# Optimization experiments

Hardware: AMD Instinct MI355X
Metric: run time of the kernel (lower is better)

The kernel has to match this reference:

```python
import jax, jax.numpy as jnp
from jax import lax
import numpy as np

B, N_VARS, M_CLAUSES, K_DIM = 1024, 64, 256, 12
MAX_ITER = 12


def setup_inputs() -> dict:
    key = jax.random.key(0)
    k1, k2, k3, k4 = jax.random.split(key, 4)
    z = jax.random.uniform(k1, (B, N_VARS), dtype=jnp.float32)          # input probabilities
    S = jax.random.normal(k2, (M_CLAUSES, N_VARS + 1), dtype=jnp.float32) * 0.2  # learnable clause matrix (col 0 = truth var)
    w = jax.random.uniform(k3, (M_CLAUSES,), dtype=jnp.float32)          # learnable clause weights
    r = jax.random.normal(k4, (B, N_VARS, K_DIM), dtype=jnp.float32)     # random init directions
    return {"z": z, "S": S, "w": w, "r": r, "max_iter": MAX_ITER}


def _mixing(z, S, w, r, max_iter):
    Bsz, n = z.shape
    m, N = S.shape  # N = n + 1 (truth variable is column 0)
    k = r.shape[-1]
    eps = jnp.float32(1e-8)

    # truth direction v_T = e_0
    vT = jnp.zeros((k,), dtype=z.dtype).at[0].set(1.0)

    # random unit directions orthogonal to v_T (zero out component along e_0)
    r_perp = r.at[..., 0].set(0.0)
    r_perp = r_perp / jnp.maximum(jnp.linalg.norm(r_perp, axis=-1, keepdims=True), eps)

    # SATNet init: v_i = -cos(pi z_i) v_T + sin(pi z_i) r_perp_i
    ang = jnp.pi * z
    Vvars = -jnp.cos(ang)[..., None] * vT + jnp.sin(ang)[..., None] * r_perp  # [B,n,k]
    V = jnp.concatenate([jnp.broadcast_to(vT, (Bsz, 1, k)), Vvars], axis=1)   # [B,N,k]

    Sw = S * w[:, None]                       # weighted clause matrix [m,N]
    W = jnp.einsum('mn,bnk->bmk', Sw, V)      # running product Sw @ V, [B,m,k]
    snrm = jnp.sum(Sw * Sw, axis=0)           # ||s_i||^2 per variable, [N]

    def coord_step(carry, i):
        V, W = carry
        s_i = Sw[:, i]                         # [m]
        v_old = V[:, i, :]                     # [B,k]
        g = jnp.einsum('bmk,m->bk', W, s_i) - snrm[i] * v_old
        v_new = -g / jnp.maximum(jnp.linalg.norm(g, axis=-1, keepdims=True), eps)
        W = W + (v_new - v_old)[:, None, :] * s_i[None, :, None]  # rank-1 update
        V = V.at[:, i, :].set(v_new)
        return (V, W), None

    def sweep(carry, _):
        carry, _ = lax.scan(coord_step, carry, jnp.arange(1, N))  # coordinate descent over variables
        return carry, None

    (V, _), _ = lax.scan(sweep, (V, W), None, length=max_iter)

    # output probabilities: z_i = arccos(-v_i . v_T) / pi
    cos = jnp.clip(-V[:, 1:, 0], -1.0 + 1e-6, 1.0 - 1e-6)
    return jnp.arccos(cos) / jnp.pi


def reference(z, S, w, r, max_iter):
    return _mixing(z, S, w, r, max_iter)
```

## Files before the change

kernel.cpp:

```cpp
#include <hip/hip_runtime.h>
#include <math.h>

#define BATCH 1024
#define NV    64
#define MC    256
#define KD    12
#define PI_F  3.14159265358979323846f

#define C0OFF  4096
#define DGAOFF 4160
#define DGBOFF 4224
#define CBUF   4288

typedef float f2  __attribute__((ext_vector_type(2)));
typedef float v4f __attribute__((ext_vector_type(4)));
typedef __attribute__((address_space(3))) float lds_f;

template <int CTRL>
__device__ __forceinline__ float dpp_addf(float x) {
  int y = __builtin_amdgcn_update_dpp(0, __float_as_int(x), CTRL, 0xF, 0xF, true);
  return x + __int_as_float(y);
}
__device__ __forceinline__ float readlane63(float x) {
  return __int_as_float(__builtin_amdgcn_readlane(__float_as_int(x), 63));
}
__device__ __forceinline__ float rlane(float x, int i) {
  return __int_as_float(__builtin_amdgcn_readlane(__float_as_int(x), i));
}

template <int IMM>
__device__ __forceinline__ void dsr(v4f& d, unsigned base) {
  asm volatile("ds_read_b128 %0, %1 offset:%2" : "=v"(d) : "v"(base), "i"(IMM));
}

__global__ void compute_C_kernel(const float* __restrict__ S,
                                 const float* __restrict__ w,
                                 float* __restrict__ Cg, int nsplit) {
  const int q = blockIdx.x;
  const int mc = blockIdx.y;
  const int j = threadIdx.x;
  if (j > NV) return;
  const int v = (q + 1) % 64 + 1;
  const int mlen = MC / nsplit;
  const int m0 = mc * mlen;
  float a0 = 0.f, a1 = 0.f, a2 = 0.f, a3 = 0.f;
  for (int m = m0; m < m0 + mlen; m += 4) {
    const float w0 = w[m], w1 = w[m + 1], w2 = w[m + 2], w3 = w[m + 3];
    a0 = fmaf(S[(m + 0) * (NV + 1) + v] * w0 * w0, S[(m + 0) * (NV + 1) + j], a0);
    a1 = fmaf(S[(m + 1) * (NV + 1) + v] * w1 * w1, S[(m + 1) * (NV + 1) + j], a1);
    a2 = fmaf(S[(m + 2) * (NV + 1) + v] * w2 * w2, S[(m + 2) * (NV + 1) + j], a2);
    a3 = fmaf(S[(m + 3) * (NV + 1) + v] * w3 * w3, S[(m + 3) * (NV + 1) + j], a3);
  }
  const float acc = (a0 + a1) + (a2 + a3);
  float* buf = Cg + mc * CBUF;
  const int p1 = (v == 1) ? 64 : (v - 1);
  const int p2 = (v == 1) ? 63 : (v == 2) ? 64 : (v - 2);
  if (j == 0) buf[C0OFF + q] = acc;
  if (j == p1) buf[DGAOFF + (v - 1)] = acc;
  if (j == p2) buf[DGBOFF + (v - 1)] = acc;
  if (j > 0) {
    const int j0 = j - 1;
    const float st = (j == v || j == p1 || j == p2) ? 0.f : acc;
    buf[q * 64 + (j0 & 7) * 8 + (j0 >> 3)] = st;
  }
}

__global__ __launch_bounds__(256, 1) void mixing_kernel(
    const float* __restrict__ z, const float* __restrict__ r,
    const float* __restrict__ Cg, const int* __restrict__ max_iter_p,
    float* __restrict__ out, int nsplit) {
  __shared__ __align__(16) float Ls[CBUF];

  const int t = threadIdx.x;
  const int l = t & 63;
  const int jgx = (l & 3) | ((l >> 1) & 4);
  const int kl = ((l >> 2) & 1) | ((l >> 3) & 6);
  const int b = blockIdx.x * 4 + (t >> 6);
  const int max_iter = max_iter_p[0];

  {
    const float4* src = (const float4*)Cg;
    float4* dst = (float4*)Ls;
    for (int idx = t; idx < CBUF / 4; idx += 256) {
      float4 a = src[idx];
      for (int u = 1; u < nsplit; ++u) {
        const float4 p = src[u * (CBUF / 4) + idx];
        a.x += p.x; a.y += p.y; a.z += p.z; a.w += p.w;
      }
      dst[idx] = a;
    }
  }

  const float my_e0 = (kl == 0) ? 1.f : 0.f;

  f2 Vv[8];
  #pragma unroll
  for (int m = 0; m < 8; ++m) {
    const int j0 = jgx + 8 * m;
    const float zv = z[b * NV + j0];
    f2 rp = {0.f, 0.f};
    if (kl < 6) rp = *(const f2*)&r[(b * NV + j0) * KD + 2 * kl];
    if (kl == 0) rp.x = 0.f;
    float ssp = fmaf(rp.x, rp.x, rp.y * rp.y);
    ssp += __shfl_xor(ssp, 4, 64);
    ssp += __shfl_xor(ssp, 16, 64);
    ssp += __shfl_xor(ssp, 32, 64);
    const float inv = 1.f / fmaxf(sqrtf(ssp), 1e-8f);
    const float sn = __builtin_amdgcn_sinf(0.5f * zv);
    const float cs = __builtin_amdgcn_cosf(0.5f * zv);
    const float si = sn * inv;
    Vv[m].x = (kl == 0) ? -cs : si * rp.x;
    Vv[m].y = si * rp.y;
  }

  __syncthreads();

  const float t0v = Ls[C0OFF + l];
  const float t1v = Ls[DGAOFF + l];
  const float t2v = Ls[DGBOFF + l];

  f2 P, vp1, vp2;

  {
    const v4f cA = *(const v4f*)&Ls[63 * 64 + jgx * 8];
    const v4f cB = *(const v4f*)&Ls[63 * 64 + jgx * 8 + 4];
    f2 q = (f2){cA.x, cA.x} * Vv[0];
    q = __builtin_elementwise_fma((f2){cA.y, cA.y}, Vv[1], q);
    q = __builtin_elementwise_fma((f2){cA.z, cA.z}, Vv[2], q);
    q = __builtin_elementwise_fma((f2){cA.w, cA.w}, Vv[3], q);
    q = __builtin_elementwise_fma((f2){cB.x, cB.x}, Vv[4], q);
    q = __builtin_elementwise_fma((f2){cB.y, cB.y}, Vv[5], q);
    q = __builtin_elementwise_fma((f2){cB.z, cB.z}, Vv[6], q);
    q = __builtin_elementwise_fma((f2){cB.w, cB.w}, Vv[7], q);
    q.x = dpp_addf<0xB1>(q.x);  q.y = dpp_addf<0xB1>(q.y);
    q.x = dpp_addf<0x4E>(q.x);  q.y = dpp_addf<0x4E>(q.y);
    q.x = dpp_addf<0x128>(q.x); q.y = dpp_addf<0x128>(q.y);
    q.x = fmaf(my_e0, Ls[C0OFF + 63], q.x);
    P = q;
    vp1.x = __shfl(Vv[7].x, (l & 0x34) | 0x0B, 64);
    vp1.y = __shfl(Vv[7].y, (l & 0x34) | 0x0B, 64);
    vp2.x = __shfl(Vv[7].x, (l & 0x34) | 0x0A, 64);
    vp2.y = __shfl(Vv[7].y, (l & 0x34) | 0x0A, 64);
  }

  const unsigned lbase = (unsigned)(unsigned long long)(lds_f*)&Ls[jgx * 8];

  v4f Rb[4][2];

#define PFROW(R) \
  dsr<((((R) & 63) * 256) + 0)>(Rb[(R) & 3][0], lbase); \
  dsr<((((R) & 63) * 256) + 16)>(Rb[(R) & 3][1], lbase);

#define WAITR(SL) \
  asm volatile("s_waitcnt lgkmcnt(4)" : "+v"(Rb[SL][0]), "+v"(Rb[SL][1]));

#define STEPF(I) { \
  constexpr int i_ = (I); \
  constexpr int s_ = i_ & 3; \
  constexpr int j0w_ = (i_ + 63) & 63; \
  constexpr int m_ = j0w_ >> 3; \
  constexpr int jgo_ = j0w_ & 7; \
  WAITR(s_) \
  PFROW(i_ + 3) \
  const float da_ = rlane(t1v, i_); \
  const float db_ = rlane(t2v, i_); \
  const float c0_ = rlane(t0v, i_); \
   \
  f2 g_; \
  g_.x = fmaf(da_, vp1.x, fmaf(db_, vp2.x, P.x)); \
  g_.y = fmaf(da_, vp1.y, fmaf(db_, vp2.y, P.y)); \
  float t_ = fmaf(g_.x, g_.x, g_.y * g_.y); \
  const v4f ceA = Rb[s_][0], ceB = Rb[s_][1]; \
  f2 q_ = (f2){ceA.x, ceA.x} * Vv[0]; \
  q_ = __builtin_elementwise_fma((f2){ceA.y, ceA.y}, Vv[1], q_); \
  t_ = dpp_addf<0x124>(t_);             \
  q_ = __builtin_elementwise_fma((f2){ceA.z, ceA.z}, Vv[2], q_); \
  q_ = __builtin_elementwise_fma((f2){ceA.w, ceA.w}, Vv[3], q_); \
  t_ = dpp_addf<0x142>(t_);             \
  q_ = __builtin_elementwise_fma((f2){ceB.x, ceB.x}, Vv[4], q_); \
  q_ = __builtin_elementwise_fma((f2){ceB.y, ceB.y}, Vv[5], q_); \
  t_ = dpp_addf<0x143>(t_);             \
  q_ = __builtin_elementwise_fma((f2){ceB.z, ceB.z}, Vv[6], q_); \
  q_ = __builtin_elementwise_fma((f2){ceB.w, ceB.w}, Vv[7], q_); \
  const float n2_ = readlane63(t_); \
  const float inv_ = __builtin_amdgcn_rsqf(fmaxf(n2_, 1e-16f)); \
  q_.x = dpp_addf<0xB1>(q_.x);  q_.y = dpp_addf<0xB1>(q_.y); \
  f2 vn_; vn_.x = -g_.x * inv_; vn_.y = -g_.y * inv_; \
  q_.x = dpp_addf<0x4E>(q_.x);  q_.y = dpp_addf<0x4E>(q_.y); \
  q_.x = dpp_addf<0x128>(q_.x); q_.y = dpp_addf<0x128>(q_.y); \
  q_.x = fmaf(my_e0, c0_, q_.x); \
   \
  Vv[m_].x = (jgx == jgo_) ? vp1.x : Vv[m_].x; \
  Vv[m_].y = (jgx == jgo_) ? vp1.y : Vv[m_].y; \
   \
  vp2 = vp1; vp1 = vn_; P = q_; \
}

#define S4(N) STEPF((N) + 0) STEPF((N) + 1) STEPF((N) + 2) STEPF((N) + 3)
#define S16(N) S4((N) + 0) S4((N) + 4) S4((N) + 8) S4((N) + 12)

  asm volatile("s_waitcnt lgkmcnt(0)" ::: "memory");
  PFROW(0) PFROW(1) PFROW(2)

  #pragma unroll 1
  for (int it = 0; it < max_iter; ++it) {
    S16(0) S16(16) S16(32) S16(48)
  }

  Vv[7].x = (jgx == 7) ? vp1.x : Vv[7].x;
  Vv[7].y = (jgx == 7) ? vp1.y : Vv[7].y;

  asm volatile("s_waitcnt lgkmcnt(0)" ::: "memory");
  __syncthreads();
  {
    float* Lw = Ls + (t >> 6) * 64;
    if (kl == 0) {
      #pragma unroll
      for (int m = 0; m < 8; ++m) Lw[jgx + 8 * m] = Vv[m].x;
    }
    __builtin_amdgcn_s_waitcnt(0);
    float cv = -Lw[l];
    cv = fminf(fmaxf(cv, -1.f + 1e-6f), 1.f - 1e-6f);
    out[b * NV + l] = acosf(cv) * (1.f / PI_F);
  }
}

extern "C" void kernel_launch(void* const* d_in, const int* in_sizes, int n_in,
                              void* d_out, int out_size, void* d_ws, size_t ws_size,
                              hipStream_t stream) {
  const float* z = (const float*)d_in[0];
  const float* S = (const float*)d_in[1];
  const float* w = (const float*)d_in[2];
  const float* r = (const float*)d_in[3];
  const int* max_iter = (const int*)d_in[4];
  float* Cg = (float*)d_ws;

  const int nsplit = (ws_size >= (size_t)8 * CBUF * 4) ? 8
                   : (ws_size >= (size_t)4 * CBUF * 4) ? 4 : 1;
  compute_C_kernel<<<dim3(NV, nsplit), 128, 0, stream>>>(S, w, Cg, nsplit);
  mixing_kernel<<<BATCH / 4, 256, 0, stream>>>(z, r, Cg, max_iter,
                                               (float*)d_out, nsplit);
}
```

Measured before the change: 141.7 us.

## Process two batch elements per wavefront to interleave independent dependency chains

Each wavefront now carries two independent batch problems (A and B) through the coordinate-descent sweep, with their steps interleaved. Blocks shrink from 4 to 2 wavefronts while the grid stays the same. The aim is to hide latency in the serial chain (readlane, rsq, DPP reductions) by giving the scheduler independent work, and to reuse each LDS row read for both problems. The cost is roughly double the VGPR use per wave and half as many waves in flight.

Result: slower. 192.4 us (+35.8%).

```diff
diff --git a/kernel.cpp b/kernel.cpp
--- a/kernel.cpp
+++ b/kernel.cpp
@@ -15,6 +15,11 @@
 typedef float f2  __attribute__((ext_vector_type(2)));
 typedef float v4f __attribute__((ext_vector_type(4)));
 typedef __attribute__((address_space(3))) float lds_f;
+
+__device__ __forceinline__ f2 bc2(float x) { f2 y; y.x = x; y.y = x; return y; }
+__device__ __forceinline__ f2 fma2(f2 a, f2 b, f2 c) {
+  return __builtin_elementwise_fma(a, b, c);
+}
 
 template <int CTRL>
 __device__ __forceinline__ float dpp_addf(float x) {
@@ -65,7 +70,7 @@
   }
 }
 
-__global__ __launch_bounds__(256, 1) void mixing_kernel(
+__global__ __launch_bounds__(128, 1) void mixing_kernel(
     const float* __restrict__ z, const float* __restrict__ r,
     const float* __restrict__ Cg, const int* __restrict__ max_iter_p,
     float* __restrict__ out, int nsplit) {
@@ -75,13 +80,14 @@
   const int l = t & 63;
   const int jgx = (l & 3) | ((l >> 1) & 4);
   const int kl = ((l >> 2) & 1) | ((l >> 3) & 6);
-  const int b = blockIdx.x * 4 + (t >> 6);
+  const int bA = blockIdx.x * 4 + (t >> 6) * 2;
+  const int bB = bA + 1;
   const int max_iter = max_iter_p[0];
 
   {
     const float4* src = (const float4*)Cg;
     float4* dst = (float4*)Ls;
-    for (int idx = t; idx < CBUF / 4; idx += 256) {
+    for (int idx = t; idx < CBUF / 4; idx += 128) {
       float4 a = src[idx];
       for (int u = 1; u < nsplit; ++u) {
         const float4 p = src[u * (CBUF / 4) + idx];
@@ -93,24 +99,30 @@
 
   const float my_e0 = (kl == 0) ? 1.f : 0.f;
 
-  f2 Vv[8];
+  f2 VvA[8], VvB[8];
   #pragma unroll
   for (int m = 0; m < 8; ++m) {
     const int j0 = jgx + 8 * m;
-    const float zv = z[b * NV + j0];
-    f2 rp = {0.f, 0.f};
-    if (kl < 6) rp = *(const f2*)&r[(b * NV + j0) * KD + 2 * kl];
-    if (kl == 0) rp.x = 0.f;
-    float ssp = fmaf(rp.x, rp.x, rp.y * rp.y);
-    ssp += __shfl_xor(ssp, 4, 64);
-    ssp += __shfl_xor(ssp, 16, 64);
-    ssp += __shfl_xor(ssp, 32, 64);
-    const float inv = 1.f / fmaxf(sqrtf(ssp), 1e-8f);
-    const float sn = __builtin_amdgcn_sinf(0.5f * zv);
-    const float cs = __builtin_amdgcn_cosf(0.5f * zv);
-    const float si = sn * inv;
-    Vv[m].x = (kl == 0) ? -cs : si * rp.x;
-    Vv[m].y = si * rp.y;
+    #pragma unroll
+    for (int ab = 0; ab < 2; ++ab) {
+      const int b = ab ? bB : bA;
+      const float zv = z[b * NV + j0];
+      f2 rp = bc2(0.f);
+      if (kl < 6) rp = *(const f2*)&r[(b * NV + j0) * KD + 2 * kl];
+      if (kl == 0) rp.x = 0.f;
+      float ssp = fmaf(rp.x, rp.x, rp.y * rp.y);
+      ssp += __shfl_xor(ssp, 4, 64);
+      ssp += __shfl_xor(ssp, 16, 64);
+      ssp += __shfl_xor(ssp, 32, 64);
+      const float inv = 1.f / fmaxf(sqrtf(ssp), 1e-8f);
+      const float sn = __builtin_amdgcn_sinf(0.5f * zv);
+      const float cs = __builtin_amdgcn_cosf(0.5f * zv);
+      const float si = sn * inv;
+      f2 vv;
+      vv.x = (kl == 0) ? -cs : si * rp.x;
+      vv.y = si * rp.y;
+      if (ab) VvB[m] = vv; else VvA[m] = vv;
+    }
   }
 
   __syncthreads();
@@ -119,28 +131,35 @@
   const float t1v = Ls[DGAOFF + l];
   const float t2v = Ls[DGBOFF + l];
 
-  f2 P, vp1, vp2;
+  f2 PA, PB, vp1A, vp1B, vp2A, vp2B;
 
   {
     const v4f cA = *(const v4f*)&Ls[63 * 64 + jgx * 8];
     const v4f cB = *(const v4f*)&Ls[63 * 64 + jgx * 8 + 4];
-    f2 q = (f2){cA.x, cA.x} * Vv[0];
-    q = __builtin_elementwise_fma((f2){cA.y, cA.y}, Vv[1], q);
-    q = __builtin_elementwise_fma((f2){cA.z, cA.z}, Vv[2], q);
-    q = __builtin_elementwise_fma((f2){cA.w, cA.w}, Vv[3], q);
-    q = __builtin_elementwise_fma((f2){cB.x, cB.x}, Vv[4], q);
-    q = __builtin_elementwise_fma((f2){cB.y, cB.y}, Vv[5], q);
-    q = __builtin_elementwise_fma((f2){cB.z, cB.z}, Vv[6], q);
-    q = __builtin_elementwise_fma((f2){cB.w, cB.w}, Vv[7], q);
-    q.x = dpp_addf<0xB1>(q.x);  q.y = dpp_addf<0xB1>(q.y);
-    q.x = dpp_addf<0x4E>(q.x);  q.y = dpp_addf<0x4E>(q.y);
-    q.x = dpp_addf<0x128>(q.x); q.y = dpp_addf<0x128>(q.y);
-    q.x = fmaf(my_e0, Ls[C0OFF + 63], q.x);
-    P = q;
-    vp1.x = __shfl(Vv[7].x, (l & 0x34) | 0x0B, 64);
-    vp1.y = __shfl(Vv[7].y, (l & 0x34) | 0x0B, 64);
-    vp2.x = __shfl(Vv[7].x, (l & 0x34) | 0x0A, 64);
-    vp2.y = __shfl(Vv[7].y, (l & 0x34) | 0x0A, 64);
+    const float c063 = Ls[C0OFF + 63];
+    #pragma unroll
+    for (int ab = 0; ab < 2; ++ab) {
+      f2* Vv = ab ? VvB : VvA;
+      f2 q = bc2(cA.x) * Vv[0];
+      q = fma2(bc2(cA.y), Vv[1], q);
+      q = fma2(bc2(cA.z), Vv[2], q);
+      q = fma2(bc2(cA.w), Vv[3], q);
+      q = fma2(bc2(cB.x), Vv[4], q);
+      q = fma2(bc2(cB.y), Vv[5], q);
+      q = fma2(bc2(cB.z), Vv[6], q);
+      q = fma2(bc2(cB.w), Vv[7], q);
+      q.x = dpp_addf<0xB1>(q.x);  q.y = dpp_addf<0xB1>(q.y);
+      q.x = dpp_addf<0x4E>(q.x);  q.y = dpp_addf<0x4E>(q.y);
+      q.x = dpp_addf<0x128>(q.x); q.y = dpp_addf<0x128>(q.y);
+      q.x = fmaf(my_e0, c063, q.x);
+      f2 v1, v2;
+      v1.x = __shfl(Vv[7].x, (l & 0x34) | 0x0B, 64);
+      v1.y = __shfl(Vv[7].y, (l & 0x34) | 0x0B, 64);
+      v2.x = __shfl(Vv[7].x, (l & 0x34) | 0x0A, 64);
+      v2.y = __shfl(Vv[7].y, (l & 0x34) | 0x0A, 64);
+      if (ab) { PB = q; vp1B = v1; vp2B = v2; }
+      else    { PA = q; vp1A = v1; vp2A = v2; }
+    }
   }
 
   const unsigned lbase = (unsigned)(unsigned long long)(lds_f*)&Ls[jgx * 8];
@@ -166,34 +185,59 @@
   const float db_ = rlane(t2v, i_); \
   const float c0_ = rlane(t0v, i_); \
    \
-  f2 g_; \
-  g_.x = fmaf(da_, vp1.x, fmaf(db_, vp2.x, P.x)); \
-  g_.y = fmaf(da_, vp1.y, fmaf(db_, vp2.y, P.y)); \
-  float t_ = fmaf(g_.x, g_.x, g_.y * g_.y); \
+  f2 gA_, gB_; \
+  gA_.x = fmaf(da_, vp1A.x, fmaf(db_, vp2A.x, PA.x)); \
+  gB_.x = fmaf(da_, vp1B.x, fmaf(db_, vp2B.x, PB.x)); \
+  gA_.y = fmaf(da_, vp1A.y, fmaf(db_, vp2A.y, PA.y)); \
+  gB_.y = fmaf(da_, vp1B.y, fmaf(db_, vp2B.y, PB.y)); \
+  float tA_ = fmaf(gA_.x, gA_.x, gA_.y * gA_.y); \
+  float tB_ = fmaf(gB_.x, gB_.x, gB_.y * gB_.y); \
   const v4f ceA = Rb[s_][0], ceB = Rb[s_][1]; \
-  f2 q_ = (f2){ceA.x, ceA.x} * Vv[0]; \
-  q_ = __builtin_elementwise_fma((f2){ceA.y, ceA.y}, Vv[1], q_); \
-  t_ = dpp_addf<0x124>(t_);             \
-  q_ = __builtin_elementwise_fma((f2){ceA.z, ceA.z}, Vv[2], q_); \
-  q_ = __builtin_elementwise_fma((f2){ceA.w, ceA.w}, Vv[3], q_); \
-  t_ = dpp_addf<0x142>(t_);             \
-  q_ = __builtin_elementwise_fma((f2){ceB.x, ceB.x}, Vv[4], q_); \
-  q_ = __builtin_elementwise_fma((f2){ceB.y, ceB.y}, Vv[5], q_); \
-  t_ = dpp_addf<0x143>(t_);             \
-  q_ = __builtin_elementwise_fma((f2){ceB.z, ceB.z}, Vv[6], q_); \
-  q_ = __builtin_elementwise_fma((f2){ceB.w, ceB.w}, Vv[7], q_); \
-  const float n2_ = readlane63(t_); \
-  const float inv_ = __builtin_amdgcn_rsqf(fmaxf(n2_, 1e-16f)); \
-  q_.x = dpp_addf<0xB1>(q_.x);  q_.y = dpp_addf<0xB1>(q_.y); \
-  f2 vn_; vn_.x = -g_.x * inv_; vn_.y = -g_.y * inv_; \
-  q_.x = dpp_addf<0x4E>(q_.x);  q_.y = dpp_addf<0x4E>(q_.y); \
-  q_.x = dpp_addf<0x128>(q_.x); q_.y = dpp_addf<0x128>(q_.y); \
-  q_.x = fmaf(my_e0, c0_, q_.x); \
+  f2 qA_ = bc2(ceA.x) * VvA[0]; \
+  f2 qB_ = bc2(ceA.x) * VvB[0]; \
+  qA_ = fma2(bc2(ceA.y), VvA[1], qA_); \
+  qB_ = fma2(bc2(ceA.y), VvB[1], qB_); \
+  tA_ = dpp_addf<0x124>(tA_); \
+  tB_ = dpp_addf<0x124>(tB_); \
+  qA_ = fma2(bc2(ceA.z), VvA[2], qA_); \
+  qB_ = fma2(bc2(ceA.z), VvB[2], qB_); \
+  qA_ = fma2(bc2(ceA.w), VvA[3], qA_); \
+  qB_ = fma2(bc2(ceA.w), VvB[3], qB_); \
+  tA_ = dpp_addf<0x142>(tA_); \
+  tB_ = dpp_addf<0x142>(tB_); \
+  qA_ = fma2(bc2(ceB.x), VvA[4], qA_); \
+  qB_ = fma2(bc2(ceB.x), VvB[4], qB_); \
+  qA_ = fma2(bc2(ceB.y), VvA[5], qA_); \
+  qB_ = fma2(bc2(ceB.y), VvB[5], qB_); \
+  tA_ = dpp_addf<0x143>(tA_); \
+  tB_ = dpp_addf<0x143>(tB_); \
+  qA_ = fma2(bc2(ceB.z), VvA[6], qA_); \
+  qB_ = fma2(bc2(ceB.z), VvB[6], qB_); \
+  qA_ = fma2(bc2(ceB.w), VvA[7], qA_); \
+  qB_ = fma2(bc2(ceB.w), VvB[7], qB_); \
+  const float n2A_ = readlane63(tA_); \
+  const float n2B_ = readlane63(tB_); \
+  const float invA_ = __builtin_amdgcn_rsqf(fmaxf(n2A_, 1e-16f)); \
+  const float invB_ = __builtin_amdgcn_rsqf(fmaxf(n2B_, 1e-16f)); \
+  qA_.x = dpp_addf<0xB1>(qA_.x);  qA_.y = dpp_addf<0xB1>(qA_.y); \
+  qB_.x = dpp_addf<0xB1>(qB_.x);  qB_.y = dpp_addf<0xB1>(qB_.y); \
+  f2 vnA_, vnB_; \
+  vnA_.x = -gA_.x * invA_; vnA_.y = -gA_.y * invA_; \
+  vnB_.x = -gB_.x * invB_; vnB_.y = -gB_.y * invB_; \
+  qA_.x = dpp_addf<0x4E>(qA_.x);  qA_.y = dpp_addf<0x4E>(qA_.y); \
+  qB_.x = dpp_addf<0x4E>(qB_.x);  qB_.y = dpp_addf<0x4E>(qB_.y); \
+  qA_.x = dpp_addf<0x128>(qA_.x); qA_.y = dpp_addf<0x128>(qA_.y); \
+  qB_.x = dpp_addf<0x128>(qB_.x); qB_.y = dpp_addf<0x128>(qB_.y); \
+  qA_.x = fmaf(my_e0, c0_, qA_.x); \
+  qB_.x = fmaf(my_e0, c0_, qB_.x); \
    \
-  Vv[m_].x = (jgx == jgo_) ? vp1.x : Vv[m_].x; \
-  Vv[m_].y = (jgx == jgo_) ? vp1.y : Vv[m_].y; \
+  VvA[m_].x = (jgx == jgo_) ? vp1A.x : VvA[m_].x; \
+  VvA[m_].y = (jgx == jgo_) ? vp1A.y : VvA[m_].y; \
+  VvB[m_].x = (jgx == jgo_) ? vp1B.x : VvB[m_].x; \
+  VvB[m_].y = (jgx == jgo_) ? vp1B.y : VvB[m_].y; \
    \
-  vp2 = vp1; vp1 = vn_; P = q_; \
+  vp2A = vp1A; vp1A = vnA_; PA = qA_; \
+  vp2B = vp1B; vp1B = vnB_; PB = qB_; \
 }
 
 #define S4(N) STEPF((N) + 0) STEPF((N) + 1) STEPF((N) + 2) STEPF((N) + 3)
@@ -207,21 +251,29 @@
     S16(0) S16(16) S16(32) S16(48)
   }
 
-  Vv[7].x = (jgx == 7) ? vp1.x : Vv[7].x;
-  Vv[7].y = (jgx == 7) ? vp1.y : Vv[7].y;
+  VvA[7].x = (jgx == 7) ? vp1A.x : VvA[7].x;
+  VvA[7].y = (jgx == 7) ? vp1A.y : VvA[7].y;
+  VvB[7].x = (jgx == 7) ? vp1B.x : VvB[7].x;
+  VvB[7].y = (jgx == 7) ? vp1B.y : VvB[7].y;
 
   asm volatile("s_waitcnt lgkmcnt(0)" ::: "memory");
   __syncthreads();
   {
-    float* Lw = Ls + (t >> 6) * 64;
+    float* Lw = Ls + (t >> 6) * 128;
     if (kl == 0) {
       #pragma unroll
-      for (int m = 0; m < 8; ++m) Lw[jgx + 8 * m] = Vv[m].x;
+      for (int m = 0; m < 8; ++m) {
+        Lw[jgx + 8 * m] = VvA[m].x;
+        Lw[64 + jgx + 8 * m] = VvB[m].x;
+      }
     }
     __builtin_amdgcn_s_waitcnt(0);
-    float cv = -Lw[l];
-    cv = fminf(fmaxf(cv, -1.f + 1e-6f), 1.f - 1e-6f);
-    out[b * NV + l] = acosf(cv) * (1.f / PI_F);
+    float cvA = -Lw[l];
+    float cvB = -Lw[64 + l];
+    cvA = fminf(fmaxf(cvA, -1.f + 1e-6f), 1.f - 1e-6f);
+    cvB = fminf(fmaxf(cvB, -1.f + 1e-6f), 1.f - 1e-6f);
+    out[bA * NV + l] = acosf(cvA) * (1.f / PI_F);
+    out[bB * NV + l] = acosf(cvB) * (1.f / PI_F);
   }
 }
 
@@ -238,6 +290,6 @@
   const int nsplit = (ws_size >= (size_t)8 * CBUF * 4) ? 8
                    : (ws_size >= (size_t)4 * CBUF * 4) ? 4 : 1;
   compute_C_kernel<<<dim3(NV, nsplit), 128, 0, stream>>>(S, w, Cg, nsplit);
-  mixing_kernel<<<BATCH / 4, 256, 0, stream>>>(z, r, Cg, max_iter,
+  mixing_kernel<<<BATCH / 4, 128, 0, stream>>>(z, r, Cg, max_iter,
                                                (float*)d_out, nsplit);
 }
```
